# Kernel tuning notes

Measured on AMD Instinct MI355X. Metric: run time of the kernel, lower is better.

Reference implementation:

```python
import jax, jax.numpy as jnp
import numpy as np

D = 384; NH = 4; FF = 1024; NL = 2
L_ENC = 750; T_AUD = 1500; VOCAB = 60; T_TXT = 256; B = 8; S_SPK = 8; GAMA = 1.0


def _conv1d(x, w, b, stride):
    y = jax.lax.conv_general_dilated(x, w, (stride,), [(1, 1)], dimension_numbers=("NCH", "OIH", "NCH"))
    return y + b[None, :, None]


def _ln(x, g, b):
    m = x.mean(-1, keepdims=True)
    v = ((x - m) ** 2).mean(-1, keepdims=True)
    return (x - m) * jax.lax.rsqrt(v + 1e-5) * g + b


def _enc_layer(x, qkv_w, qkv_b, ow, ob, f1w, f1b, f2w, f2b, g1, b1, g2, b2):
    Bq, L, d = x.shape
    hd = d // NH
    q, k, v = jnp.split(x @ qkv_w.T + qkv_b, 3, axis=-1)
    q = q.reshape(Bq, L, NH, hd); k = k.reshape(Bq, L, NH, hd); v = v.reshape(Bq, L, NH, hd)
    s = jnp.einsum("blhd,bmhd->bhlm", q, k) * np.float32(1.0 / np.sqrt(hd))
    a = jax.nn.softmax(s, axis=-1)
    ctx = jnp.einsum("bhlm,bmhd->blhd", a, v).reshape(Bq, L, d)
    x = _ln(x + ctx @ ow.T + ob, g1, b1)
    h = jax.nn.relu(x @ f1w.T + f1b) @ f2w.T + f2b
    return _ln(x + h, g2, b2)


def _gru(x, h, wih, whh, bih, bhh):
    gi = x @ wih.T + bih
    gh = h @ whh.T + bhh
    ir, iz, inn = jnp.split(gi, 3, axis=-1)
    hr, hz, hn = jnp.split(gh, 3, axis=-1)
    r = jax.nn.sigmoid(ir + hr)
    z = jax.nn.sigmoid(iz + hz)
    n = jnp.tanh(inn + r * hn)
    return (1.0 - z) * n + z * h


def _nll(logits, tgt):
    # torch F.nll_loss applied to raw scores (faithful to source), ignore_index=-100
    valid = (tgt != -100)
    idx = jnp.where(valid, tgt, 0)
    picked = jnp.take_along_axis(logits, idx[..., None], axis=-1)[..., 0]
    return -(picked * valid).sum() / jnp.maximum(valid.sum(), 1).astype(logits.dtype)


def _forward(fl, target_asr_ids, target_diar_ids, remat=False):
    (input_features, speaker_inventory, conv1_w, conv1_b, conv2_w, conv2_b,
     asr_qkv_w, asr_qkv_b, asr_attn_out_w, asr_attn_out_b, asr_ff1_w, asr_ff1_b,
     asr_ff2_w, asr_ff2_b, asr_ln1_g, asr_ln1_b, asr_ln2_g, asr_ln2_b,
     diar_qkv_w, diar_qkv_b, diar_attn_out_w, diar_attn_out_b, diar_ff1_w, diar_ff1_b,
     diar_ff2_w, diar_ff2_b, diar_ln1_g, diar_ln1_b, diar_ln2_g, diar_ln2_b,
     la_q_w, la_k_w, la_v_w, la_in_b, la_out_w, la_out_b, emb,
     asr_rnn_w_ih, asr_rnn_w_hh, asr_rnn_b_ih, asr_rnn_b_hh,
     diar_rnn_w_ih, diar_rnn_w_hh, diar_rnn_b_ih, diar_rnn_b_hh,
     asr_out_w, asr_out_b, d2a_w, d2a_b, h2a_w, h2a_b) = fl
    x = jax.nn.relu(_conv1d(input_features, conv1_w, conv1_b, 1))
    x = jax.nn.relu(_conv1d(x, conv2_w, conv2_b, 2))
    x = jnp.transpose(x, (0, 2, 1))  # [B, L_ENC, D]
    enc_asr = x
    for l in range(NL):
        enc_asr = _enc_layer(enc_asr, asr_qkv_w[l], asr_qkv_b[l], asr_attn_out_w[l], asr_attn_out_b[l],
                             asr_ff1_w[l], asr_ff1_b[l], asr_ff2_w[l], asr_ff2_b[l],
                             asr_ln1_g[l], asr_ln1_b[l], asr_ln2_g[l], asr_ln2_b[l])
    enc_diar = x
    for l in range(NL):
        enc_diar = _enc_layer(enc_diar, diar_qkv_w[l], diar_qkv_b[l], diar_attn_out_w[l], diar_attn_out_b[l],
                              diar_ff1_w[l], diar_ff1_b[l], diar_ff2_w[l], diar_ff2_b[l],
                              diar_ln1_g[l], diar_ln1_b[l], diar_ln2_g[l], diar_ln2_b[l])
    Bsz = x.shape[0]
    inv_norm = jnp.linalg.norm(speaker_inventory, axis=2)  # [B, S]

    def step(carry, tgt):
        token, asr_ctx, h_asr, h_diar, attns = carry
        e = emb[token]  # [B, D]
        h_asr = _gru(jnp.concatenate([asr_ctx, e], 1), h_asr,
                     asr_rnn_w_ih, asr_rnn_w_hh, asr_rnn_b_ih, asr_rnn_b_hh)
        # 1-dim MultiheadAttention: q=h_asr[:,:,None], k=prev attentions, v=enc_asr (vdim=384->1)
        q = h_asr[:, :, None] * la_q_w[0, 0] + la_in_b[0]   # [B, L, 1]
        k = attns * la_k_w[0, 0] + la_in_b[1]               # [B, L, 1]
        v = enc_asr @ la_v_w.T + la_in_b[2]                 # [B, L, 1]
        s = q @ jnp.swapaxes(k, 1, 2)                       # [B, L, L]; head_dim=1 -> scale 1
        a = jax.nn.softmax(s, axis=-1)
        attns_new = (a @ v) * la_out_w[0, 0] + la_out_b[0]  # [B, L, 1]
        w = attns_new[..., 0]
        asr_ctx_new = jnp.einsum("bld,bl->bd", enc_asr, w)
        spk_ctx = jnp.einsum("bld,bl->bd", enc_diar, w)
        h_diar_new = _gru(jnp.concatenate([spk_ctx, e], 1), h_diar,
                          diar_rnn_w_ih, diar_rnn_w_hh, diar_rnn_b_ih, diar_rnn_b_hh)
        sc = jnp.einsum("bsd,bd->bs", speaker_inventory, h_diar_new)
        hn = jnp.linalg.norm(h_diar_new, axis=1, keepdims=True)
        beta = jax.nn.softmax(sc / (hn * inv_norm), axis=1)
        spk_state = jnp.einsum("bsd,bs->bd", speaker_inventory, beta)
        logits = (asr_ctx_new + h_asr @ h2a_w.T + h2a_b + spk_state @ d2a_w.T + d2a_b) @ asr_out_w.T + asr_out_b
        next_tok = jnp.where(tgt == -100, 0, tgt)
        return (next_tok, asr_ctx_new, h_asr, h_diar_new, attns_new), (logits, beta)

    step_fn = jax.checkpoint(step) if remat else step
    init = (jnp.zeros((Bsz,), jnp.int32),
            jnp.zeros((Bsz, D), jnp.float32),
            jnp.zeros((Bsz, L_ENC), jnp.float32),
            jnp.zeros((Bsz, D), jnp.float32),
            jnp.zeros((Bsz, L_ENC, 1), jnp.float32))
    _, (logits_seq, beta_seq) = jax.lax.scan(step_fn, init, jnp.swapaxes(target_asr_ids, 0, 1))
    asr_outputs = jnp.swapaxes(logits_seq, 0, 1)   # [B, T, VOCAB]
    diar_outputs = jnp.swapaxes(beta_seq, 0, 1)    # [B, T, S]
    loss = _nll(asr_outputs, target_asr_ids) + GAMA * _nll(diar_outputs, target_diar_ids)
    return asr_outputs, diar_outputs, loss


def setup_inputs() -> dict:
    key = jax.random.key(0)
    cnt = [0]
    def p(shape, scale=0.05):
        cnt[0] += 1
        return jax.random.normal(jax.random.fold_in(key, cnt[0]), shape, dtype=jnp.float32) * scale
    inp = {}
    inp["input_features"] = p((B, 80, T_AUD), 1.0)
    inp["speaker_inventory"] = p((B, S_SPK, D), 1.0)
    inp["conv1_w"] = p((D, 80, 3)); inp["conv1_b"] = p((D,))
    inp["conv2_w"] = p((D, D, 3)); inp["conv2_b"] = p((D,))
    for pre in ("asr", "diar"):
        inp[pre + "_qkv_w"] = p((NL, 3 * D, D)); inp[pre + "_qkv_b"] = p((NL, 3 * D))
        inp[pre + "_attn_out_w"] = p((NL, D, D)); inp[pre + "_attn_out_b"] = p((NL, D))
        inp[pre + "_ff1_w"] = p((NL, FF, D)); inp[pre + "_ff1_b"] = p((NL, FF))
        inp[pre + "_ff2_w"] = p((NL, D, FF)); inp[pre + "_ff2_b"] = p((NL, D))
        inp[pre + "_ln1_g"] = jnp.ones((NL, D), jnp.float32); inp[pre + "_ln1_b"] = jnp.zeros((NL, D), jnp.float32)
        inp[pre + "_ln2_g"] = jnp.ones((NL, D), jnp.float32); inp[pre + "_ln2_b"] = jnp.zeros((NL, D), jnp.float32)
    inp["la_q_w"] = p((1, 1), 1.0); inp["la_k_w"] = p((1, 1), 1.0); inp["la_v_w"] = p((1, D))
    inp["la_in_b"] = p((3,)); inp["la_out_w"] = p((1, 1), 1.0); inp["la_out_b"] = p((1,))
    inp["emb"] = p((VOCAB, D), 1.0)
    inp["asr_rnn_w_ih"] = p((3 * L_ENC, 2 * D)); inp["asr_rnn_w_hh"] = p((3 * L_ENC, L_ENC))
    inp["asr_rnn_b_ih"] = p((3 * L_ENC,)); inp["asr_rnn_b_hh"] = p((3 * L_ENC,))
    inp["diar_rnn_w_ih"] = p((3 * D, 2 * D)); inp["diar_rnn_w_hh"] = p((3 * D, D))
    inp["diar_rnn_b_ih"] = p((3 * D,)); inp["diar_rnn_b_hh"] = p((3 * D,))
    inp["asr_out_w"] = p((VOCAB, D)); inp["asr_out_b"] = p((VOCAB,))
    inp["d2a_w"] = p((D, D)); inp["d2a_b"] = p((D,))
    inp["h2a_w"] = p((D, L_ENC)); inp["h2a_b"] = p((D,))
    inp["target_asr_ids"] = jax.random.randint(jax.random.fold_in(key, 9001), (B, T_TXT), 0, VOCAB, dtype=jnp.int32)
    inp["target_diar_ids"] = jax.random.randint(jax.random.fold_in(key, 9002), (B, T_TXT), 0, S_SPK, dtype=jnp.int32)
    return inp


def reference(input_features, speaker_inventory, conv1_w, conv1_b, conv2_w, conv2_b,
              asr_qkv_w, asr_qkv_b, asr_attn_out_w, asr_attn_out_b, asr_ff1_w, asr_ff1_b,
              asr_ff2_w, asr_ff2_b, asr_ln1_g, asr_ln1_b, asr_ln2_g, asr_ln2_b,
              diar_qkv_w, diar_qkv_b, diar_attn_out_w, diar_attn_out_b, diar_ff1_w, diar_ff1_b,
              diar_ff2_w, diar_ff2_b, diar_ln1_g, diar_ln1_b, diar_ln2_g, diar_ln2_b,
              la_q_w, la_k_w, la_v_w, la_in_b, la_out_w, la_out_b, emb,
              asr_rnn_w_ih, asr_rnn_w_hh, asr_rnn_b_ih, asr_rnn_b_hh,
              diar_rnn_w_ih, diar_rnn_w_hh, diar_rnn_b_ih, diar_rnn_b_hh,
              asr_out_w, asr_out_b, d2a_w, d2a_b, h2a_w, h2a_b,
              target_asr_ids, target_diar_ids):
    fl = (input_features, speaker_inventory, conv1_w, conv1_b, conv2_w, conv2_b,
          asr_qkv_w, asr_qkv_b, asr_attn_out_w, asr_attn_out_b, asr_ff1_w, asr_ff1_b,
          asr_ff2_w, asr_ff2_b, asr_ln1_g, asr_ln1_b, asr_ln2_g, asr_ln2_b,
          diar_qkv_w, diar_qkv_b, diar_attn_out_w, diar_attn_out_b, diar_ff1_w, diar_ff1_b,
          diar_ff2_w, diar_ff2_b, diar_ln1_g, diar_ln1_b, diar_ln2_g, diar_ln2_b,
          la_q_w, la_k_w, la_v_w, la_in_b, la_out_w, la_out_b, emb,
          asr_rnn_w_ih, asr_rnn_w_hh, asr_rnn_b_ih, asr_rnn_b_hh,
          diar_rnn_w_ih, diar_rnn_w_hh, diar_rnn_b_ih, diar_rnn_b_hh,
          asr_out_w, asr_out_b, d2a_w, d2a_b, h2a_w, h2a_b)
    return _forward(fl, target_asr_ids, target_diar_ids, remat=False)
```

## Files before the change

kernel.cpp:

```cpp
#include <hip/hip_runtime.h>
#include <math.h>

#define L_ENC 750
#define T_AUD 1500
#define DD    384
#define FF    1024
#define NHH   4
#define HDIM  96
#define VOCAB 60
#define T_TXT 256
#define BB    8
#define NB    480
#define TB    512

static __device__ __forceinline__ float sigmf(float x){ return 1.f/(1.f + __expf(-x)); }

static __device__ __forceinline__ float cld(const float* p){
  return __hip_atomic_load(p, __ATOMIC_RELAXED, __HIP_MEMORY_SCOPE_AGENT);
}
static __device__ __forceinline__ void cst(float* p, float v){
  __hip_atomic_store(p, v, __ATOMIC_RELAXED, __HIP_MEMORY_SCOPE_AGENT);
}

static constexpr size_t O_X  = 0;
static constexpr size_t O_EA = 2304000;
static constexpr size_t O_ED = 4608000;
static constexpr size_t O_ST = 6912000;
static constexpr size_t oHASR = O_ST + 0;
static constexpr size_t oATT0 = O_ST + 6000;
static constexpr size_t oATT1 = O_ST + 12000;
static constexpr size_t oHD   = O_ST + 18000;
static constexpr size_t oACTX = O_ST + 21072;
static constexpr size_t oSCTX = O_ST + 27216;
static constexpr size_t oPREP = O_ST + 33360;
static constexpr size_t oGIA  = O_ST + 39504;
static constexpr size_t oGHA  = O_ST + 57504;
static constexpr size_t oGID  = O_ST + 75504;
static constexpr size_t oGHD  = O_ST + 84720;
static constexpr size_t oLACC = O_ST + 93936;
static constexpr size_t oVLA  = O_ST + 93944;
static constexpr size_t oINVN = O_ST + 99944;
static constexpr size_t oBAR  = O_ST + 100008;
static constexpr size_t oZ384 = O_ST + 104200;
static constexpr size_t O_SCR = O_ST + 105000;
static constexpr size_t oWIHAT_A = O_SCR + 0;
static constexpr size_t oWHHT_A  = O_SCR + 864000;
static constexpr size_t oWIHAT_D = O_SCR + 2556000;
static constexpr size_t oWHHT_D  = O_SCR + 2998368;
static constexpr size_t oH2AT    = O_SCR + 3440736;
static constexpr size_t oAOT     = O_SCR + 3728736;
static constexpr size_t oEMBT    = O_SCR + 3751776;
static constexpr size_t oGEA     = O_SCR + 4538208;
static constexpr size_t oGED     = O_SCR + 9146208;
static constexpr size_t oDIB     = O_SCR + 11505504;

__global__ void transpose_k(const float* __restrict__ in, int ldin, int R, int C,
                            float* __restrict__ out){
  __shared__ float t[32][33];
  int c0 = blockIdx.x*32, r0 = blockIdx.y*32;
  int x = threadIdx.x, y = threadIdx.y;
  for (int i = y; i < 32; i += 8){
    int r = r0 + i, c = c0 + x;
    t[i][x] = (r < R && c < C) ? in[(size_t)r*ldin + c] : 0.f;
  }
  __syncthreads();
  for (int i = y; i < 32; i += 8){
    int c = c0 + i, r = r0 + x;
    if (c < C && r < R) out[(size_t)c*R + r] = t[x][i];
  }
}

__global__ void packT_k(const float* __restrict__ in, int ldin, int R, int K,
                        float* __restrict__ out){
  __shared__ float tl[32][33];
  int k0 = blockIdx.x*32, r0 = blockIdx.y*32;
  int x = threadIdx.x, y = threadIdx.y;
  int K4 = ((K + 3) >> 2) << 2;
  for (int i = y; i < 32; i += 8){
    int r = r0 + i, k = k0 + x;
    tl[i][x] = (r < R && k < K) ? in[(size_t)r*ldin + k] : 0.f;
  }
  __syncthreads();
  for (int i = y; i < 32; i += 8){
    int k = k0 + i, r = r0 + x;
    if (k < K4 && r < R) out[((size_t)(k >> 2)*R + r)*4 + (k & 3)] = tl[x][i];
  }
}

__global__ void kt_k(const float* __restrict__ QKV, float* __restrict__ KT){
  __shared__ float t[32][33];
  int z = blockIdx.z; int b = z >> 2, h = z & 3;
  const float* in = QKV + (size_t)b*L_ENC*1152 + 384 + h*HDIM;
  float* out = KT + (size_t)z*HDIM*L_ENC;
  int c0 = blockIdx.x*32, r0 = blockIdx.y*32;
  int x = threadIdx.x, y = threadIdx.y;
  for (int i = y; i < 32; i += 8){
    int r = r0 + i, c = c0 + x;
    t[i][x] = (r < L_ENC && c < HDIM) ? in[(size_t)r*1152 + c] : 0.f;
  }
  __syncthreads();
  for (int i = y; i < 32; i += 8){
    int c = c0 + i, r = r0 + x;
    if (c < HDIM && r < L_ENC) out[(size_t)c*L_ENC + r] = t[x][i];
  }
}

template<int RELU, int HASRES>
__global__ __launch_bounds__(256) void gemm_k(
    const float* __restrict__ A, int lda, const float* __restrict__ W, int ldw,
    const float* __restrict__ bias, const float* __restrict__ Res,
    float* __restrict__ C, int ldc, int M, int N, int K)
{
  __shared__ __align__(16) float As[16][132];
  __shared__ __align__(16) float Ws[16][68];
  int tid = threadIdx.x;
  int row0 = blockIdx.y*128, col0 = blockIdx.x*64;
  int tx = tid & 15, ty = tid >> 4;
  int lr = tid >> 2, lk = (tid & 3)*4;
  float acc[8][4] = {};
  for (int k0 = 0; k0 < K; k0 += 16){
    float4 a0 = make_float4(0,0,0,0), a1 = make_float4(0,0,0,0), w0 = make_float4(0,0,0,0);
    int r0i = row0 + lr, r1i = row0 + 64 + lr, wri = col0 + lr;
    if (r0i < M) a0 = *(const float4*)(A + (size_t)r0i*lda + k0 + lk);
    if (r1i < M) a1 = *(const float4*)(A + (size_t)r1i*lda + k0 + lk);
    if (wri < N) w0 = *(const float4*)(W + (size_t)wri*ldw + k0 + lk);
    As[lk+0][lr] = a0.x; As[lk+1][lr] = a0.y; As[lk+2][lr] = a0.z; As[lk+3][lr] = a0.w;
    As[lk+0][64+lr] = a1.x; As[lk+1][64+lr] = a1.y; As[lk+2][64+lr] = a1.z; As[lk+3][64+lr] = a1.w;
    Ws[lk+0][lr] = w0.x; Ws[lk+1][lr] = w0.y; Ws[lk+2][lr] = w0.z; Ws[lk+3][lr] = w0.w;
    __syncthreads();
    #pragma unroll
    for (int k = 0; k < 16; k++){
      float4 b4 = *(const float4*)&Ws[k][tx*4];
      float4 a4 = *(const float4*)&As[k][ty*8];
      float4 a5 = *(const float4*)&As[k][ty*8+4];
      acc[0][0] += a4.x*b4.x; acc[0][1] += a4.x*b4.y; acc[0][2] += a4.x*b4.z; acc[0][3] += a4.x*b4.w;
      acc[1][0] += a4.y*b4.x; acc[1][1] += a4.y*b4.y; acc[1][2] += a4.y*b4.z; acc[1][3] += a4.y*b4.w;
      acc[2][0] += a4.z*b4.x; acc[2][1] += a4.z*b4.y; acc[2][2] += a4.z*b4.z; acc[2][3] += a4.z*b4.w;
      acc[3][0] += a4.w*b4.x; acc[3][1] += a4.w*b4.y; acc[3][2] += a4.w*b4.z; acc[3][3] += a4.w*b4.w;
      acc[4][0] += a5.x*b4.x; acc[4][1] += a5.x*b4.y; acc[4][2] += a5.x*b4.z; acc[4][3] += a5.x*b4.w;
      acc[5][0] += a5.y*b4.x; acc[5][1] += a5.y*b4.y; acc[5][2] += a5.y*b4.z; acc[5][3] += a5.y*b4.w;
      acc[6][0] += a5.z*b4.x; acc[6][1] += a5.z*b4.y; acc[6][2] += a5.z*b4.z; acc[6][3] += a5.z*b4.w;
      acc[7][0] += a5.w*b4.x; acc[7][1] += a5.w*b4.y; acc[7][2] += a5.w*b4.z; acc[7][3] += a5.w*b4.w;
    }
    __syncthreads();
  }
  #pragma unroll
  for (int ii = 0; ii < 8; ii++){
    int m = row0 + ty*8 + ii;
    if (m >= M) continue;
    #pragma unroll
    for (int jj = 0; jj < 4; jj++){
      int n = col0 + tx*4 + jj;
      if (n >= N) continue;
      float v = acc[ii][jj] + bias[n];
      if (HASRES) v += Res[(size_t)m*ldc + n];
      if (RELU) v = fmaxf(v, 0.f);
      C[(size_t)m*ldc + n] = v;
    }
  }
}

__global__ void im2col1(const float* __restrict__ in, float* __restrict__ P){
  int t = blockIdx.x, b = blockIdx.y, i = threadIdx.x;
  if (i >= 240) return;
  int ic = i/3, kt = i - ic*3;
  int p = t + kt - 1;
  P[((size_t)(b*T_AUD + t))*240 + i] = (p >= 0 && p < T_AUD) ? in[((size_t)(b*80 + ic))*T_AUD + p] : 0.f;
}

// ... 72 lines not shown
    if (lane == 0) den_s[wv] = den;
  }
  __syncthreads();
  if (i < L_ENC){
    float idn = 1.f/den_s[wv];
    const float* vb = QKV + (size_t)b*L_ENC*1152 + 768 + h*HDIM;
    float a0 = 0.f, a1 = 0.f;
    for (int j = 0; j < L_ENC; j++){
      float pj = p_s[wv][j];
      const float* vr = vb + (size_t)j*1152;
      a0 += pj*vr[lane];
      if (lane < 32) a1 += pj*vr[lane + 64];
    }
    size_t ob = ((size_t)(b*L_ENC + i))*DD + h*HDIM;
    ctx[ob + lane] = a0*idn;
    if (lane < 32) ctx[ob + lane + 64] = a1*idn;
  }
}

__global__ __launch_bounds__(384) void embed_k(const float* __restrict__ emb,
    const int* __restrict__ tgtA, float* __restrict__ E){
  int row = blockIdx.x; int t = row >> 3, b = row & 7;
  int tok = 0;
  if (t > 0){ int v = tgtA[b*T_TXT + t - 1]; tok = (v == -100) ? 0 : v; }
  E[(size_t)row*DD + threadIdx.x] = emb[(size_t)tok*DD + threadIdx.x];
}

__global__ __launch_bounds__(256) void vla_k(const float* __restrict__ EA,
    const float* __restrict__ lav, const float* __restrict__ lain, float* __restrict__ VLA){
  int row = blockIdx.x*4 + (threadIdx.x >> 6);
  int lane = threadIdx.x & 63;
  if (row >= BB*L_ENC) return;
  const float* p = EA + (size_t)row*DD;
  float s = 0.f;
  for (int d = lane; d < DD; d += 64) s += p[d]*lav[d];
  #pragma unroll
  for (int o = 32; o > 0; o >>= 1) s += __shfl_xor(s, o);
  if (lane == 0) VLA[row] = s + lain[2];
}

__global__ void invn_k(const float* __restrict__ inv, float* __restrict__ INVN){
  int row = blockIdx.x; int lane = threadIdx.x;
  float s = 0.f;
  for (int d = lane; d < DD; d += 64){ float v = inv[(size_t)row*DD + d]; s += v*v; }
  #pragma unroll
  for (int o = 32; o > 0; o >>= 1) s += __shfl_xor(s, o);
  if (lane == 0) INVN[row] = sqrtf(s);
}

struct DecParams {
  float* ws; float* out;
  const float* ABHH; const float* DBHH;
  const float* SPK;  const float* AOB;
  const float* LAQ; const float* LAK; const float* LAIB; const float* LAOW; const float* LAOB;
  const float* H2AB; const float* D2AB;
  const int* TGTA; const int* TGTD;
};

static __device__ __forceinline__ void gbar(unsigned* s, unsigned epoch){
  __syncthreads();
  int tid = threadIdx.x;
  if (blockIdx.x == 0){
    if (tid > 0 && tid < NB){
      while (__hip_atomic_load(&s[tid*4], __ATOMIC_RELAXED, __HIP_MEMORY_SCOPE_AGENT) < epoch)
        __builtin_amdgcn_s_sleep(4);
    }
    __syncthreads();
    if (tid < NB)
      __hip_atomic_store(&s[(512 + tid)*4], epoch, __ATOMIC_RELAXED, __HIP_MEMORY_SCOPE_AGENT);
  } else {
    if (tid == 0){
      __hip_atomic_store(&s[blockIdx.x*4], epoch, __ATOMIC_RELAXED, __HIP_MEMORY_SCOPE_AGENT);
      while (__hip_atomic_load(&s[(512 + blockIdx.x)*4], __ATOMIC_RELAXED, __HIP_MEMORY_SCOPE_AGENT) < epoch)
        __builtin_amdgcn_s_sleep(4);
    }
    __syncthreads();
  }
}

#define FMA8(acc, s_, base) { const float4 b0_ = *(const float4*)&(base)[0]; const float4 b1_ = *(const float4*)&(base)[4]; \
  acc[0]+=b0_.x*(s_); acc[1]+=b0_.y*(s_); acc[2]+=b0_.z*(s_); acc[3]+=b0_.w*(s_); \
  acc[4]+=b1_.x*(s_); acc[5]+=b1_.y*(s_); acc[6]+=b1_.z*(s_); acc[7]+=b1_.w*(s_); }

template<int NR, int KH, int KQH>
__device__ void gates_fn(int task, const float* __restrict__ WIT, const float* __restrict__ WHT,
                         const float* __restrict__ ctxv, const float* __restrict__ hv,
                         const float* __restrict__ GE, const float* __restrict__ bhh,
                         float* __restrict__ GI, float* __restrict__ GH, int t, float* SM)
{
  float* ac  = SM;
  float* hh  = SM + 3072;
  float* pgi = SM + 3072 + KQH*32;
  float* pgh = pgi + 4096;
  int tid = threadIdx.x;
  for (int idx = tid; idx < 3072; idx += TB){ int b = idx/384, k = idx - b*384; ac[k*8+b] = cld(&ctxv[idx]); }
  for (int idx = tid; idx < KH*8;  idx += TB){ int b = idx/KH,  k = idx - b*KH;  hh[k*8+b] = cld(&hv[idx]); }
  for (int idx = KH*8 + tid; idx < KQH*32; idx += TB) hh[idx] = 0.f;
  __syncthreads();
  int rl = tid & 7, kp = tid >> 3;
  int r = task*8 + rl;
  float gi[8] = {}, gh[8] = {};
  if (r < NR){
    const float4* W4 = (const float4*)WIT;
    int q0 = (kp*96) >> 6, q1 = ((kp+1)*96) >> 6;
    for (int q = q0; q < q1; q++){
      float4 w4 = W4[(size_t)q*NR + r];
      const float* a = &ac[q*32];
      FMA8(gi, w4.x, a+0); FMA8(gi, w4.y, a+8); FMA8(gi, w4.z, a+16); FMA8(gi, w4.w, a+24);
    }
    const float4* WH4 = (const float4*)WHT;
    int h0 = (kp*KQH) >> 6, h1 = ((kp+1)*KQH) >> 6;
    for (int q = h0; q < h1; q++){
      float4 w4 = WH4[(size_t)q*NR + r];
      const float* a = &hh[q*32];
      FMA8(gh, w4.x, a+0); FMA8(gh, w4.y, a+8); FMA8(gh, w4.z, a+16); FMA8(gh, w4.w, a+24);
    }
  }
  #pragma unroll
  for (int b = 0; b < 8; b++){ pgi[(kp*8+rl)*8 + b] = gi[b]; pgh[(kp*8+rl)*8 + b] = gh[b]; }
  __syncthreads();
  if (tid < 64){
    int rl2 = tid & 7, bb = tid >> 3;
    int rr = task*8 + rl2;
    if (rr < NR){
      float s1 = 0.f, s2 = 0.f;
      #pragma unroll 8
      for (int kq = 0; kq < 64; kq++){ s1 += pgi[(kq*8+rl2)*8+bb]; s2 += pgh[(kq*8+rl2)*8+bb]; }
      cst(&GI[(size_t)bb*NR + rr], s1 + GE[((size_t)t*8 + bb)*NR + rr]);
      cst(&GH[(size_t)bb*NR + rr], s2 + bhh[rr]);
    }
  }
  __syncthreads();
}

__device__ void phase_hattn_ctx(int bid, int t, float* ws, const DecParams& P, float* SM)
{
  float* kk = SM;
  float* vv = SM + 768;
  float* wl = SM + 1536;
  float* hl = SM + 1552;
  float* part = SM + 1568;
  int tid = threadIdx.x;
  int b = bid & 7, chunk = bid >> 3;
  int i0 = chunk*13; int n = L_ENC - i0; if (n > 13) n = 13;
  const float* acur = ws + ((t & 1) ? oATT1 : oATT0);
  float*       anxt = ws + ((t & 1) ? oATT0 : oATT1);
  const float* GIAp = ws + oGIA; const float* GHAp = ws + oGHA;
  float* HASRp = ws + oHASR;
  const float* VLAp = ws + oVLA;
  float kw = P.LAK[0], kb = P.LAIB[1];
  for (int j = tid; j < L_ENC; j += TB){
    kk[j] = cld(&acur[b*L_ENC + j])*kw + kb;
    vv[j] = VLAp[b*L_ENC + j];
  }
  __syncthreads();
  int wv = tid >> 6, lane = tid & 63;
  float laq = P.LAQ[0], li0 = P.LAIB[0], low = P.LAOW[0], lob = P.LAOB[0];
  for (int il = wv; il < n; il += 8){
    int i = i0 + il;
    int base = b*2250 + i;
    float rr = sigmf(cld(&GIAp[base]) + cld(&GHAp[base]));
    float zz = sigmf(cld(&GIAp[base+750]) + cld(&GHAp[base+750]));
    float nn = tanhf(cld(&GIAp[base+1500]) + rr*cld(&GHAp[base+1500]));
    float h = (1.f - zz)*nn + zz*cld(&HASRp[b*L_ENC + i]);
    float q = h*laq + li0;
    float sr[12]; float mx = -1e30f;
    #pragma unroll
    for (int jt = 0; jt < 12; jt++){
      int j = lane + jt*64;
      float s = (j < L_ENC) ? q*kk[j] : -1e30f;
      sr[jt] = s; mx = fmaxf(mx, s);
    }
    #pragma unroll
    for (int o = 32; o > 0; o >>= 1) mx = fmaxf(mx, __shfl_xor(mx, o));
    float se = 0.f, sv = 0.f;
    #pragma unroll
    for (int jt = 0; jt < 12; jt++){
      int j = lane + jt*64;
      if (j < L_ENC){ float e = __expf(sr[jt] - mx); se += e; sv += e*vv[j]; }
    }
    #pragma unroll
    for (int o = 32; o > 0; o >>= 1){ se += __shfl_xor(se, o); sv += __shfl_xor(sv, o); }
    if (lane == 0){
      cst(&HASRp[b*L_ENC + i], h);
      float w = (sv/se)*low + lob;
      cst(&anxt[b*L_ENC + i], w);
      wl[il] = w; hl[il] = h;
    }
  }
  __syncthreads();
  if (tid < 480){
    int lg = tid / 96, dq = tid - lg*96;
    int d0 = dq*4;
    const float* EAb = ws + O_EA + (size_t)b*L_ENC*DD + d0;
    const float* EDb = ws + O_ED + (size_t)b*L_ENC*DD + d0;
    const float* H2b = ws + oH2AT + d0;
    float4 a4 = {0,0,0,0}, s4 = {0,0,0,0}, h4 = {0,0,0,0};
    for (int j = lg; j < n; j += 5){
      size_t lo = (size_t)(i0 + j)*DD;
      float wj = wl[j], hj = hl[j];
      float4 e = *(const float4*)(EAb + lo);
      a4.x += e.x*wj; a4.y += e.y*wj; a4.z += e.z*wj; a4.w += e.w*wj;
      float4 e2 = *(const float4*)(EDb + lo);
      s4.x += e2.x*wj; s4.y += e2.y*wj; s4.z += e2.z*wj; s4.w += e2.w*wj;
      float4 e3 = *(const float4*)(H2b + lo);
      h4.x += e3.x*hj; h4.y += e3.y*hj; h4.z += e3.z*hj; h4.w += e3.w*hj;
    }
    float* pp = part + (size_t)tid*12;
    *(float4*)pp = a4; *(float4*)(pp+4) = s4; *(float4*)(pp+8) = h4;
  }
  __syncthreads();
  if (tid < 96){
    float4 ra = {0,0,0,0}, rs = {0,0,0,0}, rh = {0,0,0,0};
    #pragma unroll
    for (int g = 0; g < 5; g++){
      const float* pp = part + (size_t)(g*96 + tid)*12;
      float4 pa = *(const float4*)pp, ps = *(const float4*)(pp+4), ph = *(const float4*)(pp+8);
      ra.x += pa.x; ra.y += pa.y; ra.z += pa.z; ra.w += pa.w;
      rs.x += ps.x; rs.y += ps.y; rs.z += ps.z; rs.w += ps.w;
      rh.x += ph.x; rh.y += ph.y; rh.z += ph.z; rh.w += ph.w;
    }
    int par = t & 1;
    int d0 = tid*4;
    float* A = &ws[oACTX + par*3072 + b*DD + d0];
    float* S = &ws[oSCTX + par*3072 + b*DD + d0];
    float* Pr = &ws[oPREP + par*3072 + b*DD + d0];
    atomicAdd(&A[0], ra.x); atomicAdd(&A[1], ra.y); atomicAdd(&A[2], ra.z); atomicAdd(&A[3], ra.w);
    atomicAdd(&S[0], rs.x); atomicAdd(&S[1], rs.y); atomicAdd(&S[2], rs.z); atomicAdd(&S[3], rs.w);
    atomicAdd(&Pr[0], ra.x+rh.x); atomicAdd(&Pr[1], ra.y+rh.y);
    atomicAdd(&Pr[2], ra.z+rh.z); atomicAdd(&Pr[3], ra.w+rh.w);
  }
  __syncthreads();
}

__device__ void phase_final(int b, int t, float* ws, const float* prep,
                            const DecParams& P, float* SM)
{
  float* hd_s = SM;
  float* pre_s = SM + 384;
  float* red = SM + 768;
  float* beta_s = SM + 1280;
  float* sc_s = SM + 1288;
  float* part2 = SM + 1296;
  int tid = threadIdx.x;
  bool act = tid < DD;
  const float* GIDp = ws + oGID; const float* GHDp = ws + oGHD;
  float* HDp = ws + oHD;
  float h = 0.f;
  if (act){
    int base = b*1152 + tid;
    float rr = sigmf(cld(&GIDp[base]) + cld(&GHDp[base]));
    float zz = sigmf(cld(&GIDp[base+384]) + cld(&GHDp[base+384]));
    float nn = tanhf(cld(&GIDp[base+768]) + rr*cld(&GHDp[base+768]));
    h = (1.f - zz)*nn + zz*cld(&HDp[b*DD + tid]);
    hd_s[tid] = h; cst(&HDp[b*DD + tid], h);
  }
  red[tid] = act ? h*h : 0.f;
  __syncthreads();
  for (int s = 256; s > 0; s >>= 1){ if (tid < s) red[tid] += red[tid+s]; __syncthreads(); }
  float hn = sqrtf(red[0]);
  int sg = tid >> 6, lane = tid & 63;
  float ps = 0.f;
  for (int j = lane; j < DD; j += 64) ps += P.SPK[((size_t)(b*8 + sg))*DD + j]*hd_s[j];
  #pragma unroll
  for (int o = 32; o > 0; o >>= 1) ps += __shfl_xor(ps, o);
  if (lane == 0) sc_s[sg] = ps / (hn * ws[oINVN + b*8 + sg]);
  __syncthreads();
  if (tid == 0){
    float mx = -1e30f;
    for (int s2 = 0; s2 < 8; s2++) mx = fmaxf(mx, sc_s[s2]);
    float sm = 0.f;
    for (int s2 = 0; s2 < 8; s2++){ float e = __expf(sc_s[s2] - mx); beta_s[s2] = e; sm += e; }
    float isv = 1.f/sm;
    for (int s2 = 0; s2 < 8; s2++) beta_s[s2] *= isv;
    int td = P.TGTD[b*T_TXT + t];
    if (td != -100){ atomicAdd(&ws[oLACC+2], beta_s[td]); atomicAdd(&ws[oLACC+3], 1.f); }
  }
  __syncthreads();
  if (tid < 8) P.out[122880 + ((size_t)(b*T_TXT + t))*8 + tid] = beta_s[tid];
  if (act){
    float p = cld(&prep[b*DD + tid]);
    const float* Mb = ws + oDIB + (size_t)(b*8)*DD + tid;
    #pragma unroll
    for (int s2 = 0; s2 < 8; s2++) p += beta_s[s2]*Mb[(size_t)s2*DD];
    pre_s[tid] = p;
  }
  __syncthreads();
  {
    int vg = tid >> 6, v = tid & 63;
    float pl = 0.f;
    if (v < VOCAB){
      const float* AOTp = ws + oAOT;
      int d0 = vg*48;
      for (int d2 = d0; d2 < d0+48; d2++) pl += pre_s[d2]*AOTp[d2*VOCAB + v];
    }
    part2[vg*64 + v] = pl;
  }
  __syncthreads();
  if (tid < VOCAB){
    float lg = P.AOB[tid];
    #pragma unroll
    for (int g = 0; g < 8; g++) lg += part2[g*64 + tid];
    P.out[((size_t)(b*T_TXT + t))*VOCAB + tid] = lg;
    int ta = P.TGTA[b*T_TXT + t];
    if (ta == tid) atomicAdd(&ws[oLACC+0], lg);
    if (tid == 0 && ta != -100) atomicAdd(&ws[oLACC+1], 1.f);
  }
  __syncthreads();
}

__global__ __launch_bounds__(TB, 4) void dec_loop(DecParams P)
{
  __shared__ __align__(16) float SM[17280];
  int bid = blockIdx.x;
  float* ws = P.ws;
  unsigned* slots = (unsigned*)(ws + oBAR);
  unsigned ep = 0;

  if (bid < 282)
    gates_fn<2250,750,188>(bid, ws+oWIHAT_A, ws+oWHHT_A, ws+oACTX, ws+oHASR,
                           ws+oGEA, P.ABHH, ws+oGIA, ws+oGHA, 0, SM);
  else if (bid < 290){
    int b = bid - 282;
    for (int d = threadIdx.x; d < DD; d += TB)
      cst(&ws[oPREP + b*DD + d], P.H2AB[d] + P.D2AB[d]);
  }
  gbar(slots, ++ep);

  for (int t = 0; t <= T_TXT; t++){
    if (t < T_TXT && bid < 464) phase_hattn_ctx(bid, t, ws, P, SM);
    else if (bid >= 464 && bid < 472 && t >= 1)
      phase_final(bid - 464, t - 1, ws, ws + oPREP + ((t-1) & 1)*3072, P, SM);
    gbar(slots, ++ep);
    if (t == T_TXT) break;

    if (bid < 144)
      gates_fn<1152,384,96>(bid, ws+oWIHAT_D, ws+oWHHT_D, ws+oSCTX+(t&1)*3072, ws+oHD,
                            ws+oGED, P.DBHH, ws+oGID, ws+oGHD, t, SM);
    else if (bid < 426){
      if (t + 1 < T_TXT)
        gates_fn<2250,750,188>(bid-144, ws+oWIHAT_A, ws+oWHHT_A, ws+oACTX+(t&1)*3072, ws+oHASR,
                               ws+oGEA, P.ABHH, ws+oGIA, ws+oGHA, t+1, SM);
    } else if (bid < 434 && t + 1 < T_TXT){
      int b = bid - 426, par = (t + 1) & 1;
      for (int d = threadIdx.x; d < DD; d += TB){
        cst(&ws[oACTX + par*3072 + b*DD + d], 0.f);
        cst(&ws[oSCTX + par*3072 + b*DD + d], 0.f);
        cst(&ws[oPREP + par*3072 + b*DD + d], P.H2AB[d] + P.D2AB[d]);
      }
    }
    gbar(slots, ++ep);
  }
}

__global__ void loss_final_k(const float* __restrict__ lacc, float* __restrict__ out){
  if (threadIdx.x == 0 && blockIdx.x == 0){
    float la = lacc[0]/fmaxf(lacc[1], 1.f);
    float ld = lacc[2]/fmaxf(lacc[3], 1.f);
    out[139264] = -(la + ld);
  }
}

extern "C" void kernel_launch(void* const* d_in, const int* in_sizes, int n_in,
                              void* d_out, int out_size, void* d_ws, size_t ws_size,
                              hipStream_t stream)
{
  (void)in_sizes; (void)n_in; (void)out_size; (void)ws_size;
  float* ws  = (float*)d_ws;
  float* out = (float*)d_out;

  const float* IN0   = (const float*)d_in[0];
  const float* SPK   = (const float*)d_in[1];
  const float* C1W   = (const float*)d_in[2];
  const float* C1B   = (const float*)d_in[3];
  const float* C2W   = (const float*)d_in[4];
  const float* C2B   = (const float*)d_in[5];
  const float* LAQ   = (const float*)d_in[30];
  const float* LAK   = (const float*)d_in[31];
  const float* LAV   = (const float*)d_in[32];
  const float* LAIB  = (const float*)d_in[33];
  const float* LAOW  = (const float*)d_in[34];
  const float* LAOB  = (const float*)d_in[35];
  const float* EMB   = (const float*)d_in[36];
  const float* AWIH  = (const float*)d_in[37];
  const float* AWHH  = (const float*)d_in[38];
  const float* ABIH  = (const float*)d_in[39];
  const float* ABHH  = (const float*)d_in[40];
  const float* DWIH  = (const float*)d_in[41];
  const float* DWHH  = (const float*)d_in[42];
  const float* DBIH  = (const float*)d_in[43];
  const float* DBHH  = (const float*)d_in[44];
  const float* AOW   = (const float*)d_in[45];
  const float* AOB   = (const float*)d_in[46];
  const float* D2AW  = (const float*)d_in[47];
  const float* D2AB  = (const float*)d_in[48];
  const float* H2AW  = (const float*)d_in[49];
  const float* H2AB  = (const float*)d_in[50];
  const int*   TGTA  = (const int*)d_in[51];
  const int*   TGTD  = (const int*)d_in[52];

  const size_t S_QKV = O_SCR;
  const size_t S_KT  = O_SCR + 6912000;
  const size_t S_CTX = O_SCR + 9216000;
  const size_t S_Y   = O_SCR + 11520000;
  const size_t S_H   = O_SCR + 13824000;
  const size_t X1T   = S_KT;
  const size_t Pc1   = S_H;
  const size_t Pc2   = S_QKV;

  hipMemsetAsync((void*)(ws + O_ST), 0, 105000*sizeof(float), stream);

  im2col1<<<dim3(1500,8), 256, 0, stream>>>(IN0, ws + Pc1);
  gemm_k<1,0><<<dim3(6,94), 256, 0, stream>>>(ws+Pc1, 240, C1W, 240, C1B, nullptr, ws+X1T, 384, 12000, 384, 240);
  im2col2<<<dim3(750,8), 384, 0, stream>>>(ws+X1T, ws+Pc2);
  gemm_k<1,0><<<dim3(6,47), 256, 0, stream>>>(ws+Pc2, 1152, C2W, 1152, C2B, nullptr, ws+O_X, 384, 6000, 384, 1152);

  dup_k<<<2250, 256, 0, stream>>>(ws+O_X, ws+O_EA, ws+O_ED);

  auto enc_layer = [&](float* Xb, const float* qw, const float* qb, const float* ow,
                       const float* ob, const float* f1w, const float* f1b,
                       const float* f2w, const float* f2b,
                       const float* g1, const float* b1, const float* g2, const float* b2){
    gemm_k<0,0><<<dim3(18,47), 256, 0, stream>>>(Xb, 384, qw, 384, qb, nullptr, ws+S_QKV, 1152, 6000, 1152, 384);
    kt_k<<<dim3(3,24,32), dim3(32,8), 0, stream>>>(ws+S_QKV, ws+S_KT);
    attn_enc<<<dim3(47,4,8), 1024, 0, stream>>>(ws+S_QKV, ws+S_KT, ws+S_CTX);
    gemm_k<0,1><<<dim3(6,47), 256, 0, stream>>>(ws+S_CTX, 384, ow, 384, ob, Xb, ws+S_Y, 384, 6000, 384, 384);
    ln_k<<<6000, 128, 0, stream>>>(ws+S_Y, g1, b1);
    gemm_k<1,0><<<dim3(16,47), 256, 0, stream>>>(ws+S_Y, 384, f1w, 384, f1b, nullptr, ws+S_H, 1024, 6000, 1024, 384);
    gemm_k<0,1><<<dim3(6,47), 256, 0, stream>>>(ws+S_H, 1024, f2w, 1024, f2b, ws+S_Y, Xb, 384, 6000, 384, 1024);
    ln_k<<<6000, 128, 0, stream>>>(Xb, g2, b2);
  };
  for (int st = 0; st < 2; st++){
    int base = (st == 0) ? 6 : 18;
    float* Xb = ws + ((st == 0) ? O_EA : O_ED);
    const float* qkvw = (const float*)d_in[base+0];
    const float* qkvb = (const float*)d_in[base+1];
    const float* aow  = (const float*)d_in[base+2];
    const float* aob2 = (const float*)d_in[base+3];
    const float* f1w  = (const float*)d_in[base+4];
    const float* f1b  = (const float*)d_in[base+5];
    const float* f2w  = (const float*)d_in[base+6];
    const float* f2b  = (const float*)d_in[base+7];
    const float* g1   = (const float*)d_in[base+8];
    const float* b1   = (const float*)d_in[base+9];
    const float* g2   = (const float*)d_in[base+10];
    const float* b2   = (const float*)d_in[base+11];
    for (int l = 0; l < 2; l++){
      enc_layer(Xb, qkvw + (size_t)l*1152*384, qkvb + (size_t)l*1152,
                aow + (size_t)l*384*384, aob2 + (size_t)l*384,
                f1w + (size_t)l*1024*384, f1b + (size_t)l*1024,
                f2w + (size_t)l*384*1024, f2b + (size_t)l*384,
                g1 + (size_t)l*384, b1 + (size_t)l*384, g2 + (size_t)l*384, b2 + (size_t)l*384);
    }
  }

  packT_k<<<dim3(12,71), dim3(32,8), 0, stream>>>(AWIH, 768, 2250, 384, ws+oWIHAT_A);
  packT_k<<<dim3(24,71), dim3(32,8), 0, stream>>>(AWHH, 750, 2250, 750, ws+oWHHT_A);
  packT_k<<<dim3(12,36), dim3(32,8), 0, stream>>>(DWIH, 768, 1152, 384, ws+oWIHAT_D);
  packT_k<<<dim3(12,36), dim3(32,8), 0, stream>>>(DWHH, 384, 1152, 384, ws+oWHHT_D);
  transpose_k<<<dim3(24,12), dim3(32,8), 0, stream>>>(H2AW, 750, 384, 750, ws+oH2AT);
  transpose_k<<<dim3(12,2),  dim3(32,8), 0, stream>>>(AOW, 384, 60, 384, ws+oAOT);
  embed_k<<<2048, 384, 0, stream>>>(EMB, TGTA, ws+oEMBT);
  gemm_k<0,0><<<dim3(36,16), 256, 0, stream>>>(ws+oEMBT, 384, AWIH+384, 768, ABIH, nullptr, ws+oGEA, 2250, 2048, 2250, 384);
  gemm_k<0,0><<<dim3(18,16), 256, 0, stream>>>(ws+oEMBT, 384, DWIH+384, 768, DBIH, nullptr, ws+oGED, 1152, 2048, 1152, 384);
  gemm_k<0,0><<<dim3(6,1), 256, 0, stream>>>(SPK, 384, D2AW, 384, ws+oZ384, nullptr, ws+oDIB, 384, 64, 384, 384);
  vla_k<<<1500, 256, 0, stream>>>(ws+O_EA, LAV, LAIB, ws+oVLA);
  invn_k<<<64, 64, 0, stream>>>(SPK, ws+oINVN);

  DecParams DP;
  DP.ws = ws; DP.out = out;
  DP.ABHH = ABHH; DP.DBHH = DBHH; DP.SPK = SPK; DP.AOB = AOB;
  DP.LAQ = LAQ; DP.LAK = LAK; DP.LAIB = LAIB; DP.LAOW = LAOW; DP.LAOB = LAOB;
  DP.H2AB = H2AB; DP.D2AB = D2AB; DP.TGTA = TGTA; DP.TGTD = TGTD;
  dec_loop<<<dim3(NB), dim3(TB), 0, stream>>>(DP);

  loss_final_k<<<1, 64, 0, stream>>>(ws+oLACC, out);
}
```

Before: 21.56 ms.

## Store decoder GRU weights and encoder outputs in bf16 to halve streaming bandwidth

Converts the packed GRU weight matrices, the H2A transpose and both encoder output tensors to bf16 before the persistent decoder loop. Gate computation is rebalanced to 32 rows per block over fewer blocks, and the attention context loop reads 8 bf16 values per load. This targets the per-step memory traffic of re-reading weights and encoder states across 256 sequential steps. In exchange it loses precision in weights and activations, adds conversion kernels, and leaves fewer blocks doing gate work.

```diff
diff --git a/kernel.cpp b/kernel.cpp
--- a/kernel.cpp
+++ b/kernel.cpp
@@ -20,6 +20,15 @@
 }
 static __device__ __forceinline__ void cst(float* p, float v){
   __hip_atomic_store(p, v, __ATOMIC_RELAXED, __HIP_MEMORY_SCOPE_AGENT);
+}
+
+static __device__ __forceinline__ float bf2f(unsigned int v){
+  union { unsigned int u; float f; } c; c.u = v << 16; return c.f;
+}
+static __device__ __forceinline__ unsigned short f2bf(float x){
+  union { float f; unsigned int u; } c; c.f = x;
+  unsigned int u = c.u + 0x7fffu + ((c.u >> 16) & 1u);
+  return (unsigned short)(u >> 16);
 }
 
 static constexpr size_t O_X  = 0;
@@ -44,15 +53,18 @@
 static constexpr size_t oZ384 = O_ST + 104200;
 static constexpr size_t O_SCR = O_ST + 105000;
 static constexpr size_t oWIHAT_A = O_SCR + 0;
-static constexpr size_t oWHHT_A  = O_SCR + 864000;
-static constexpr size_t oWIHAT_D = O_SCR + 2556000;
-static constexpr size_t oWHHT_D  = O_SCR + 2998368;
-static constexpr size_t oH2AT    = O_SCR + 3440736;
-static constexpr size_t oAOT     = O_SCR + 3728736;
-static constexpr size_t oEMBT    = O_SCR + 3751776;
-static constexpr size_t oGEA     = O_SCR + 4538208;
-static constexpr size_t oGED     = O_SCR + 9146208;
-static constexpr size_t oDIB     = O_SCR + 11505504;
+static constexpr size_t oWHHT_A  = O_SCR + 432000;
+static constexpr size_t oWIHAT_D = O_SCR + 1278000;
+static constexpr size_t oWHHT_D  = O_SCR + 1499184;
+static constexpr size_t oH2ATh   = O_SCR + 1720368;
+static constexpr size_t oAOT     = O_SCR + 1864368;
+static constexpr size_t oEMBT    = O_SCR + 1887408;
+static constexpr size_t oGEA     = O_SCR + 2673840;
+static constexpr size_t oGED     = O_SCR + 7281840;
+static constexpr size_t oDIB     = O_SCR + 9641136;
+static constexpr size_t oEAh     = O_SCR + 9665712;
+static constexpr size_t oEDh     = O_SCR + 10817712;
+static constexpr size_t oTMPH    = O_SCR + 12000000;
 
 __global__ void transpose_k(const float* __restrict__ in, int ldin, int R, int C,
                             float* __restrict__ out){
@@ -70,12 +82,12 @@
   }
 }
 
-__global__ void packT_k(const float* __restrict__ in, int ldin, int R, int K,
-                        float* __restrict__ out){
+__global__ void packTbf_k(const float* __restrict__ in, int ldin, int R, int K,
+                          unsigned short* __restrict__ out){
   __shared__ float tl[32][33];
   int k0 = blockIdx.x*32, r0 = blockIdx.y*32;
   int x = threadIdx.x, y = threadIdx.y;
-  int K4 = ((K + 3) >> 2) << 2;
+  int K8 = ((K + 7) >> 3) << 3;
   for (int i = y; i < 32; i += 8){
     int r = r0 + i, k = k0 + x;
     tl[i][x] = (r < R && k < K) ? in[(size_t)r*ldin + k] : 0.f;
@@ -83,8 +95,17 @@
   __syncthreads();
   for (int i = y; i < 32; i += 8){
     int k = k0 + i, r = r0 + x;
-    if (k < K4 && r < R) out[((size_t)(k >> 2)*R + r)*4 + (k & 3)] = tl[x][i];
-  }
+    if (k < K8 && r < R) out[((size_t)(k >> 3)*R + r)*8 + (k & 7)] = f2bf(tl[x][i]);
+  }
+}
+
+__global__ __launch_bounds__(256) void cvtbf_k(const float* __restrict__ src,
+    unsigned short* __restrict__ dst, int n4){
+  int i = blockIdx.x*256 + threadIdx.x;
+  if (i >= n4) return;
+  float4 v = ((const float4*)src)[i];
+  ushort4 o; o.x = f2bf(v.x); o.y = f2bf(v.y); o.z = f2bf(v.z); o.w = f2bf(v.w);
+  ((ushort4*)dst)[i] = o;
 }
 
 __global__ void kt_k(const float* __restrict__ QKV, float* __restrict__ KT){
@@ -323,50 +344,63 @@
   acc[0]+=b0_.x*(s_); acc[1]+=b0_.y*(s_); acc[2]+=b0_.z*(s_); acc[3]+=b0_.w*(s_); \
   acc[4]+=b1_.x*(s_); acc[5]+=b1_.y*(s_); acc[6]+=b1_.z*(s_); acc[7]+=b1_.w*(s_); }
 
-template<int NR, int KH, int KQH>
-__device__ void gates_fn(int task, const float* __restrict__ WIT, const float* __restrict__ WHT,
+#define GFMA8(acc, wv_, a_) { \
+  FMA8(acc, bf2f(wv_.x & 0xffffu), (a_)+0);  FMA8(acc, bf2f(wv_.x >> 16), (a_)+8); \
+  FMA8(acc, bf2f(wv_.y & 0xffffu), (a_)+16); FMA8(acc, bf2f(wv_.y >> 16), (a_)+24); \
+  FMA8(acc, bf2f(wv_.z & 0xffffu), (a_)+32); FMA8(acc, bf2f(wv_.z >> 16), (a_)+40); \
+  FMA8(acc, bf2f(wv_.w & 0xffffu), (a_)+48); FMA8(acc, bf2f(wv_.w >> 16), (a_)+56); }
+
+#define ACC8(acc, ev_, s_) { \
+  acc[0]+=bf2f(ev_.x&0xffffu)*(s_); acc[1]+=bf2f(ev_.x>>16)*(s_); \
+  acc[2]+=bf2f(ev_.y&0xffffu)*(s_); acc[3]+=bf2f(ev_.y>>16)*(s_); \
+  acc[4]+=bf2f(ev_.z&0xffffu)*(s_); acc[5]+=bf2f(ev_.z>>16)*(s_); \
+  acc[6]+=bf2f(ev_.w&0xffffu)*(s_); acc[7]+=bf2f(ev_.w>>16)*(s_); }
+
+template<int NR, int KH, int KOH>
+__device__ void gates_fn(int task, const unsigned short* __restrict__ WIT,
+                         const unsigned short* __restrict__ WHT,
                          const float* __restrict__ ctxv, const float* __restrict__ hv,
                          const float* __restrict__ GE, const float* __restrict__ bhh,
                          float* __restrict__ GI, float* __restrict__ GH, int t, float* SM)
 {
   float* ac  = SM;
   float* hh  = SM + 3072;
-  float* pgi = SM + 3072 + KQH*32;
+  float* pgi = SM + 3072 + KOH*64;
   float* pgh = pgi + 4096;
   int tid = threadIdx.x;
   for (int idx = tid; idx < 3072; idx += TB){ int b = idx/384, k = idx - b*384; ac[k*8+b] = cld(&ctxv[idx]); }
   for (int idx = tid; idx < KH*8;  idx += TB){ int b = idx/KH,  k = idx - b*KH;  hh[k*8+b] = cld(&hv[idx]); }
-  for (int idx = KH*8 + tid; idx < KQH*32; idx += TB) hh[idx] = 0.f;
-  __syncthreads();
-  int rl = tid & 7, kp = tid >> 3;
-  int r = task*8 + rl;
+  for (int idx = KH*8 + tid; idx < KOH*64; idx += TB) hh[idx] = 0.f;
+  __syncthreads();
+  int rl = tid & 31, kp = tid >> 5;
+  int r = task*32 + rl;
   float gi[8] = {}, gh[8] = {};
   if (r < NR){
-    const float4* W4 = (const float4*)WIT;
-    int q0 = (kp*96) >> 6, q1 = ((kp+1)*96) >> 6;
-    for (int q = q0; q < q1; q++){
-      float4 w4 = W4[(size_t)q*NR + r];
-      const float* a = &ac[q*32];
-      FMA8(gi, w4.x, a+0); FMA8(gi, w4.y, a+8); FMA8(gi, w4.z, a+16); FMA8(gi, w4.w, a+24);
-    }
-    const float4* WH4 = (const float4*)WHT;
-    int h0 = (kp*KQH) >> 6, h1 = ((kp+1)*KQH) >> 6;
+    const uint4* W4 = (const uint4*)WIT;
+    #pragma unroll
+    for (int q = kp*3; q < kp*3+3; q++){
+      uint4 wq = W4[(size_t)q*NR + r];
+      const float* a = &ac[q*64];
+      GFMA8(gi, wq, a);
+    }
+    const uint4* WH4 = (const uint4*)WHT;
+    int h0 = (kp*KOH) >> 4, h1 = ((kp+1)*KOH) >> 4;
     for (int q = h0; q < h1; q++){
-      float4 w4 = WH4[(size_t)q*NR + r];
-      const float* a = &hh[q*32];
-      FMA8(gh, w4.x, a+0); FMA8(gh, w4.y, a+8); FMA8(gh, w4.z, a+16); FMA8(gh, w4.w, a+24);
+      uint4 wq = WH4[(size_t)q*NR + r];
+      const float* a = &hh[q*64];
+      GFMA8(gh, wq, a);
     }
   }
   #pragma unroll
-  for (int b = 0; b < 8; b++){ pgi[(kp*8+rl)*8 + b] = gi[b]; pgh[(kp*8+rl)*8 + b] = gh[b]; }
-  __syncthreads();
-  if (tid < 64){
-    int rl2 = tid & 7, bb = tid >> 3;
-    int rr = task*8 + rl2;
+  for (int b = 0; b < 8; b++){ pgi[(kp*32+rl)*8 + b] = gi[b]; pgh[(kp*32+rl)*8 + b] = gh[b]; }
+  __syncthreads();
+  if (tid < 256){
+    int rl2 = tid & 31, bb = tid >> 5;
+    int rr = task*32 + rl2;
     if (rr < NR){
       float s1 = 0.f, s2 = 0.f;
-      #pragma unroll 8
-      for (int kq = 0; kq < 64; kq++){ s1 += pgi[(kq*8+rl2)*8+bb]; s2 += pgh[(kq*8+rl2)*8+bb]; }
+      #pragma unroll
+      for (int kq = 0; kq < 16; kq++){ s1 += pgi[(kq*32+rl2)*8+bb]; s2 += pgh[(kq*32+rl2)*8+bb]; }
       cst(&GI[(size_t)bb*NR + rr], s1 + GE[((size_t)t*8 + bb)*NR + rr]);
       cst(&GH[(size_t)bb*NR + rr], s2 + bhh[rr]);
     }
@@ -374,7 +408,11 @@
   __syncthreads();
 }
 
-__device__ void phase_hattn_ctx(int bid, int t, float* ws, const DecParams& P, float* SM)
+__device__ void phase_hattn_ctx(int bid, int t, float* ws,
+                                const unsigned short* __restrict__ EAh,
+                                const unsigned short* __restrict__ EDh,
+                                const unsigned short* __restrict__ H2h,
+                                const DecParams& P, float* SM)
 {
   float* kk = SM;
   float* vv = SM + 768;
@@ -431,45 +469,36 @@
   }
   __syncthreads();
   if (tid < 480){
-    int lg = tid / 96, dq = tid - lg*96;
-    int d0 = dq*4;
-    const float* EAb = ws + O_EA + (size_t)b*L_ENC*DD + d0;
-    const float* EDb = ws + O_ED + (size_t)b*L_ENC*DD + d0;
-    const float* H2b = ws + oH2AT + d0;
-    float4 a4 = {0,0,0,0}, s4 = {0,0,0,0}, h4 = {0,0,0,0};
-    for (int j = lg; j < n; j += 5){
-      size_t lo = (size_t)(i0 + j)*DD;
+    int lg = tid / 48, oct = tid - lg*48;
+    int d0 = oct*8;
+    float a8[8] = {}, s8[8] = {}, h8[8] = {};
+    for (int j = lg; j < n; j += 10){
+      size_t ro = ((size_t)(b*L_ENC + i0 + j))*DD + d0;
       float wj = wl[j], hj = hl[j];
-      float4 e = *(const float4*)(EAb + lo);
-      a4.x += e.x*wj; a4.y += e.y*wj; a4.z += e.z*wj; a4.w += e.w*wj;
-      float4 e2 = *(const float4*)(EDb + lo);
-      s4.x += e2.x*wj; s4.y += e2.y*wj; s4.z += e2.z*wj; s4.w += e2.w*wj;
-      float4 e3 = *(const float4*)(H2b + lo);
-      h4.x += e3.x*hj; h4.y += e3.y*hj; h4.z += e3.z*hj; h4.w += e3.w*hj;
-    }
-    float* pp = part + (size_t)tid*12;
-    *(float4*)pp = a4; *(float4*)(pp+4) = s4; *(float4*)(pp+8) = h4;
-  }
-  __syncthreads();
-  if (tid < 96){
-    float4 ra = {0,0,0,0}, rs = {0,0,0,0}, rh = {0,0,0,0};
-    #pragma unroll
-    for (int g = 0; g < 5; g++){
-      const float* pp = part + (size_t)(g*96 + tid)*12;
-      float4 pa = *(const float4*)pp, ps = *(const float4*)(pp+4), ph = *(const float4*)(pp+8);
-      ra.x += pa.x; ra.y += pa.y; ra.z += pa.z; ra.w += pa.w;
-      rs.x += ps.x; rs.y += ps.y; rs.z += ps.z; rs.w += ps.w;
-      rh.x += ph.x; rh.y += ph.y; rh.z += ph.z; rh.w += ph.w;
+      uint4 e1 = *(const uint4*)&EAh[ro];
+      ACC8(a8, e1, wj);
+      uint4 e2 = *(const uint4*)&EDh[ro];
+      ACC8(s8, e2, wj);
+      uint4 e3 = *(const uint4*)&H2h[(size_t)(i0 + j)*DD + d0];
+      ACC8(h8, e3, hj);
+    }
+    float* pp = part + (size_t)(lg*48 + oct)*24;
+    #pragma unroll
+    for (int e = 0; e < 8; e++){ pp[e] = a8[e]; pp[8+e] = s8[e]; pp[16+e] = h8[e]; }
+  }
+  __syncthreads();
+  if (tid < DD){
+    int oct = tid >> 3, e = tid & 7;
+    float ra = 0.f, rs = 0.f, rh = 0.f;
+    #pragma unroll
+    for (int lg = 0; lg < 10; lg++){
+      const float* pp = part + (size_t)(lg*48 + oct)*24;
+      ra += pp[e]; rs += pp[8+e]; rh += pp[16+e];
     }
     int par = t & 1;
-    int d0 = tid*4;
-    float* A = &ws[oACTX + par*3072 + b*DD + d0];
-    float* S = &ws[oSCTX + par*3072 + b*DD + d0];
-    float* Pr = &ws[oPREP + par*3072 + b*DD + d0];
-    atomicAdd(&A[0], ra.x); atomicAdd(&A[1], ra.y); atomicAdd(&A[2], ra.z); atomicAdd(&A[3], ra.w);
-    atomicAdd(&S[0], rs.x); atomicAdd(&S[1], rs.y); atomicAdd(&S[2], rs.z); atomicAdd(&S[3], rs.w);
-    atomicAdd(&Pr[0], ra.x+rh.x); atomicAdd(&Pr[1], ra.y+rh.y);
-    atomicAdd(&Pr[2], ra.z+rh.z); atomicAdd(&Pr[3], ra.w+rh.w);
+    atomicAdd(&ws[oACTX + par*3072 + b*DD + tid], ra);
+    atomicAdd(&ws[oSCTX + par*3072 + b*DD + tid], rs);
+    atomicAdd(&ws[oPREP + par*3072 + b*DD + tid], ra + rh);
   }
   __syncthreads();
 }
@@ -557,33 +586,40 @@
   float* ws = P.ws;
   unsigned* slots = (unsigned*)(ws + oBAR);
   unsigned ep = 0;
-
-  if (bid < 282)
-    gates_fn<2250,750,188>(bid, ws+oWIHAT_A, ws+oWHHT_A, ws+oACTX, ws+oHASR,
-                           ws+oGEA, P.ABHH, ws+oGIA, ws+oGHA, 0, SM);
-  else if (bid < 290){
-    int b = bid - 282;
+  const unsigned short* WIA = (const unsigned short*)(ws + oWIHAT_A);
+  const unsigned short* WHA = (const unsigned short*)(ws + oWHHT_A);
+  const unsigned short* WID = (const unsigned short*)(ws + oWIHAT_D);
+  const unsigned short* WHD = (const unsigned short*)(ws + oWHHT_D);
+  const unsigned short* EAh = (const unsigned short*)(ws + oEAh);
+  const unsigned short* EDh = (const unsigned short*)(ws + oEDh);
+  const unsigned short* H2h = (const unsigned short*)(ws + oH2ATh);
+
+  if (bid < 71)
+    gates_fn<2250,750,94>(bid, WIA, WHA, ws+oACTX, ws+oHASR,
+                          ws+oGEA, P.ABHH, ws+oGIA, ws+oGHA, 0, SM);
+  else if (bid < 79){
+    int b = bid - 71;
     for (int d = threadIdx.x; d < DD; d += TB)
       cst(&ws[oPREP + b*DD + d], P.H2AB[d] + P.D2AB[d]);
   }
   gbar(slots, ++ep);
 
   for (int t = 0; t <= T_TXT; t++){
-    if (t < T_TXT && bid < 464) phase_hattn_ctx(bid, t, ws, P, SM);
+    if (t < T_TXT && bid < 464) phase_hattn_ctx(bid, t, ws, EAh, EDh, H2h, P, SM);
     else if (bid >= 464 && bid < 472 && t >= 1)
       phase_final(bid - 464, t - 1, ws, ws + oPREP + ((t-1) & 1)*3072, P, SM);
     gbar(slots, ++ep);
     if (t == T_TXT) break;
 
-    if (bid < 144)
-      gates_fn<1152,384,96>(bid, ws+oWIHAT_D, ws+oWHHT_D, ws+oSCTX+(t&1)*3072, ws+oHD,
+    if (bid < 36)
+      gates_fn<1152,384,48>(bid, WID, WHD, ws+oSCTX+(t&1)*3072, ws+oHD,
                             ws+oGED, P.DBHH, ws+oGID, ws+oGHD, t, SM);
-    else if (bid < 426){
+    else if (bid < 107){
       if (t + 1 < T_TXT)
-        gates_fn<2250,750,188>(bid-144, ws+oWIHAT_A, ws+oWHHT_A, ws+oACTX+(t&1)*3072, ws+oHASR,
-                               ws+oGEA, P.ABHH, ws+oGIA, ws+oGHA, t+1, SM);
-    } else if (bid < 434 && t + 1 < T_TXT){
-      int b = bid - 426, par = (t + 1) & 1;
+        gates_fn<2250,750,94>(bid-36, WIA, WHA, ws+oACTX+(t&1)*3072, ws+oHASR,
+                              ws+oGEA, P.ABHH, ws+oGIA, ws+oGHA, t+1, SM);
+    } else if (bid < 115 && t + 1 < T_TXT){
+      int b = bid - 107, par = (t + 1) & 1;
       for (int d = threadIdx.x; d < DD; d += TB){
         cst(&ws[oACTX + par*3072 + b*DD + d], 0.f);
         cst(&ws[oSCTX + par*3072 + b*DD + d], 0.f);
@@ -695,11 +731,12 @@
     }
   }
 
-  packT_k<<<dim3(12,71), dim3(32,8), 0, stream>>>(AWIH, 768, 2250, 384, ws+oWIHAT_A);
-  packT_k<<<dim3(24,71), dim3(32,8), 0, stream>>>(AWHH, 750, 2250, 750, ws+oWHHT_A);
-  packT_k<<<dim3(12,36), dim3(32,8), 0, stream>>>(DWIH, 768, 1152, 384, ws+oWIHAT_D);
-  packT_k<<<dim3(12,36), dim3(32,8), 0, stream>>>(DWHH, 384, 1152, 384, ws+oWHHT_D);
-  transpose_k<<<dim3(24,12), dim3(32,8), 0, stream>>>(H2AW, 750, 384, 750, ws+oH2AT);
+  packTbf_k<<<dim3(12,71), dim3(32,8), 0, stream>>>(AWIH, 768, 2250, 384, (unsigned short*)(ws+oWIHAT_A));
+  packTbf_k<<<dim3(24,71), dim3(32,8), 0, stream>>>(AWHH, 750, 2250, 750, (unsigned short*)(ws+oWHHT_A));
+  packTbf_k<<<dim3(12,36), dim3(32,8), 0, stream>>>(DWIH, 768, 1152, 384, (unsigned short*)(ws+oWIHAT_D));
+  packTbf_k<<<dim3(12,36), dim3(32,8), 0, stream>>>(DWHH, 384, 1152, 384, (unsigned short*)(ws+oWHHT_D));
+  transpose_k<<<dim3(24,12), dim3(32,8), 0, stream>>>(H2AW, 750, 384, 750, ws+oTMPH);
+  cvtbf_k<<<282, 256, 0, stream>>>(ws+oTMPH, (unsigned short*)(ws+oH2ATh), 72000);
   transpose_k<<<dim3(12,2),  dim3(32,8), 0, stream>>>(AOW, 384, 60, 384, ws+oAOT);
   embed_k<<<2048, 384, 0, stream>>>(EMB, TGTA, ws+oEMBT);
   gemm_k<0,0><<<dim3(36,16), 256, 0, stream>>>(ws+oEMBT, 384, AWIH+384, 768, ABIH, nullptr, ws+oGEA, 2250, 2048, 2250, 384);
@@ -707,6 +744,8 @@
   gemm_k<0,0><<<dim3(6,1), 256, 0, stream>>>(SPK, 384, D2AW, 384, ws+oZ384, nullptr, ws+oDIB, 384, 64, 384, 384);
   vla_k<<<1500, 256, 0, stream>>>(ws+O_EA, LAV, LAIB, ws+oVLA);
   invn_k<<<64, 64, 0, stream>>>(SPK, ws+oINVN);
+  cvtbf_k<<<2250, 256, 0, stream>>>(ws+O_EA, (unsigned short*)(ws+oEAh), 576000);
+  cvtbf_k<<<2250, 256, 0, stream>>>(ws+O_ED, (unsigned short*)(ws+oEDh), 576000);
 
   DecParams DP;
   DP.ws = ws; DP.out = out;
```

Measured after the change: 24.96 ms. 1.16x slower.
